# Kernel optimization log

Measured on AMD Instinct MI355X. Metric: run time of the kernel, lower is better.

Reference implementation:

```python
import jax, jax.numpy as jnp
import numpy as np

N = 50000
E = 800000
IN_F = 128
HID = 128
OUT_F = 64
MU = 2.0
EPS = 1e-12


def setup_inputs() -> dict:
    key = jax.random.key(0)
    ks = jax.random.split(key, 20)
    d = {}
    d["x"] = jax.random.normal(ks[0], (N, IN_F), dtype=jnp.float32)
    d["edge_src"] = jax.random.randint(ks[1], (E,), 0, N, dtype=jnp.int32)
    d["edge_dst"] = jax.random.randint(ks[2], (E,), 0, N, dtype=jnp.int32)
    d["edge_val"] = jax.random.uniform(ks[3], (E,), dtype=jnp.float32)
    # layer 0: in=128 -> pool=128 -> out=128 (activation=relu)
    s0 = 1.0 / np.sqrt(IN_F)
    d["pool_w0"] = jax.random.uniform(ks[4], (IN_F, IN_F), jnp.float32, -s0, s0)
    d["pool_b0"] = jax.random.uniform(ks[5], (IN_F,), jnp.float32, -s0, s0)
    d["fc1_w0"] = jax.random.uniform(ks[6], (HID, IN_F), jnp.float32, -s0, s0)
    d["fc1_b0"] = jax.random.uniform(ks[7], (HID,), jnp.float32, -s0, s0)
    d["fc2_w0"] = jax.random.uniform(ks[8], (HID, IN_F), jnp.float32, -s0, s0)
    d["fc2_b0"] = jax.random.uniform(ks[9], (HID,), jnp.float32, -s0, s0)
    # layer 1 (final): in=128 -> pool=128 -> out=64 (no activation)
    s1 = 1.0 / np.sqrt(HID)
    d["pool_w1"] = jax.random.uniform(ks[10], (HID, HID), jnp.float32, -s1, s1)
    d["pool_b1"] = jax.random.uniform(ks[11], (HID,), jnp.float32, -s1, s1)
    d["fc1_w1"] = jax.random.uniform(ks[12], (OUT_F, HID), jnp.float32, -s1, s1)
    d["fc1_b1"] = jax.random.uniform(ks[13], (OUT_F,), jnp.float32, -s1, s1)
    d["fc2_w1"] = jax.random.uniform(ks[14], (OUT_F, HID), jnp.float32, -s1, s1)
    d["fc2_b1"] = jax.random.uniform(ks[15], (OUT_F,), jnp.float32, -s1, s1)
    return d


def _sage_conv(x, src, dst, val, pw, pb, w1, b1, w2, b2, act):
    # L2-normalize rows (F.normalize(x, dim=1))
    xn = x / jnp.maximum(jnp.linalg.norm(x, axis=1, keepdims=True), EPS)
    h = jax.nn.relu(xn @ pw.T + pb)               # [N, pool]
    h_mu = h ** MU                                # elementwise pow
    # spmm(adj, h_mu): gather source rows, scale by edge weight, scatter-add to dst rows
    agg = jax.ops.segment_sum(h_mu[src] * val[:, None], dst, num_segments=N)
    agg = agg ** (1.0 / MU)                       # generalized-mean root
    out = (h @ w1.T + b1) + (agg @ w2.T + b2)
    return jax.nn.relu(out) if act else out


def reference(x, edge_src, edge_dst, edge_val,
              pool_w0, pool_b0, fc1_w0, fc1_b0, fc2_w0, fc2_b0,
              pool_w1, pool_b1, fc1_w1, fc1_b1, fc2_w1, fc2_b1):
    h = _sage_conv(x, edge_src, edge_dst, edge_val,
                   pool_w0, pool_b0, fc1_w0, fc1_b0, fc2_w0, fc2_b0, act=True)
    out = _sage_conv(h, edge_src, edge_dst, edge_val,
                     pool_w1, pool_b1, fc1_w1, fc1_b1, fc2_w1, fc2_b1, act=False)
    return out
```

## Files before the change

kernel.cpp:

```cpp
#include <hip/hip_runtime.h>

#define FF 128
#define BCAP 8192
#define CHUNK 4096
#define PITCH 136

typedef __attribute__((ext_vector_type(8))) short short8;
typedef __attribute__((ext_vector_type(4))) float f32x4;

__device__ __forceinline__ unsigned short bf16_rne(float f) {
    unsigned u = __float_as_uint(f);
    u += 0x7fffu + ((u >> 16) & 1u);
    return (unsigned short)(u >> 16);
}
__device__ __forceinline__ float bf16_to_f32(unsigned short h) {
    return __uint_as_float(((unsigned)h) << 16);
}

__global__ __launch_bounds__(256, 2)
void poolpartA_kernel(const float* __restrict__ x,
                      const unsigned short* __restrict__ Wh, const unsigned short* __restrict__ Wl,
                      const float* __restrict__ bias,
                      unsigned short* __restrict__ hout, unsigned short* __restrict__ hsqout,
                      const int* __restrict__ esrc, const int* __restrict__ edst,
                      const float* __restrict__ eval,
                      int* __restrict__ bucket_cnt, int2* __restrict__ ebuf,
                      int N, int E, int nchunks)
{
    __shared__ alignas(16) char smem[37888];
    const int t = threadIdx.x;

    if (blockIdx.x < nchunks) {
        int* cnt   = (int*)smem;
        int* sc    = cnt + 256;
        int* excl  = sc + 256;
        int* cur   = excl + 256;
        int* gbase = cur + 256;
        int2* staged = (int2*)(smem + 5 * 256 * 4);
        const int e0 = blockIdx.x * CHUNK;
        const int n  = min(CHUNK, E - e0);

        cnt[t] = 0;
        __syncthreads();
        for (int i = t; i < n; i += 256)
            atomicAdd(&cnt[((unsigned)edst[e0 + i]) >> 8], 1);
        __syncthreads();

        sc[t] = cnt[t];
        __syncthreads();
        #pragma unroll
        for (int off = 1; off < 256; off <<= 1) {
            int v = (t >= off) ? sc[t - off] : 0;
            __syncthreads();
            sc[t] += v;
            __syncthreads();
        }
        excl[t] = sc[t] - cnt[t];
        cur[t]  = excl[t];
        if (cnt[t] > 0) gbase[t] = atomicAdd(&bucket_cnt[t], cnt[t]);
        __syncthreads();

        for (int i = t; i < n; i += 256) {
            int d = edst[e0 + i];
            int s = esrc[e0 + i];
            float v = eval[e0 + i];
            int b = ((unsigned)d) >> 8;
            int slot = atomicAdd(&cur[b], 1);
            staged[slot] = make_int2((s & 0xffff) | (d << 16), __float_as_int(v));
        }
        __syncthreads();

        for (int p = t; p < n; p += 256) {
            int2 ent = staged[p];
            int b = ((unsigned)ent.x) >> 24;
            int gpos = gbase[b] + (p - excl[b]);
            ebuf[(size_t)b * BCAP + gpos] = ent;
        }
    } else {
        unsigned short* sX = (unsigned short*)smem;
        float* sNorm = (float*)(smem + 64 * PITCH * 2);
        unsigned short* sOutQ = (unsigned short*)(smem + 64 * PITCH * 2 + 256);
        const int tile = blockIdx.x - nchunks;

        #pragma unroll
        for (int rg = 0; rg < 2; ++rg) {
            const int row = rg * 32 + (t >> 3);
            const int c0  = (t & 7) * 16;
            const int n   = tile * 64 + row;
            const int base = row * PITCH + c0;
            float v[16];
            if (n < N) {
                const float4* p = (const float4*)(x + (size_t)n * FF + c0);
                #pragma unroll
                for (int i = 0; i < 4; ++i) {
                    float4 q = p[i];
                    v[4*i] = q.x; v[4*i+1] = q.y; v[4*i+2] = q.z; v[4*i+3] = q.w;
                }
            } else {
                #pragma unroll
                for (int i = 0; i < 16; ++i) v[i] = 0.f;
            }
            float ss = 0.f;
            #pragma unroll
            for (int i = 0; i < 16; ++i) ss = fmaf(v[i], v[i], ss);
            union { unsigned short u[8]; short8 s; } h0, h1;
            #pragma unroll
            for (int i = 0; i < 8; ++i) {
                h0.u[i] = bf16_rne(v[i]);
                h1.u[i] = bf16_rne(v[8 + i]);
            }
            *(short8*)&sX[base]     = h0.s;
            *(short8*)&sX[base + 8] = h1.s;
            ss += __shfl_xor(ss, 1);
            ss += __shfl_xor(ss, 2);
            ss += __shfl_xor(ss, 4);
            if ((t & 7) == 0) sNorm[row] = 1.0f / fmaxf(sqrtf(ss), 1e-12f);
        }
        __syncthreads();

        const int lane = t & 63, wave = t >> 6;
        const int quad = lane >> 4, l16 = lane & 15;

        short8 Bh[2][4], Bl[2][4];
        #pragma unroll
        for (int c = 0; c < 2; ++c) {
            const int jt = 2 * wave + c;
            #pragma unroll
            for (int tt = 0; tt < 4; ++tt) {
                const size_t o = ((size_t)(jt * 4 + tt) * 64 + lane) * 8;
                Bh[c][tt] = *(const short8*)&Wh[o];
                Bl[c][tt] = *(const short8*)&Wl[o];
            }
        }

        f32x4 acc[4][2];
        #pragma unroll
        for (int r = 0; r < 4; ++r)
            #pragma unroll
            for (int c = 0; c < 2; ++c) {
                f32x4 z = {0.f, 0.f, 0.f, 0.f};
                acc[r][c] = z;
            }

        #pragma unroll
        for (int tt = 0; tt < 4; ++tt) {
            short8 Ah[4];
            #pragma unroll
            for (int r = 0; r < 4; ++r)
                Ah[r] = *(const short8*)&sX[(r * 16 + l16) * PITCH + tt * 32 + quad * 8];
            #pragma unroll
            for (int c = 0; c < 2; ++c)
                #pragma unroll
                for (int r = 0; r < 4; ++r) {
                    acc[r][c] = __builtin_amdgcn_mfma_f32_16x16x32_bf16(Ah[r], Bh[c][tt], acc[r][c], 0, 0, 0);
                    acc[r][c] = __builtin_amdgcn_mfma_f32_16x16x32_bf16(Ah[r], Bl[c][tt], acc[r][c], 0, 0, 0);
                }
        }

        __syncthreads();
        #pragma unroll
        for (int c = 0; c < 2; ++c) {
            const int j = (2 * wave + c) * 16 + l16;
            const float bj = bias[j];
            #pragma unroll
            for (int r = 0; r < 4; ++r) {
                #pragma unroll
                for (int g = 0; g < 4; ++g) {
                    const int nl = r * 16 + quad * 4 + g;
                    float s = sNorm[nl];
                    float val = fmaf(acc[r][c][g], s, bj);
                    val = fmaxf(val, 0.f);
                    sX   [nl * PITCH + j] = bf16_rne(val);
                    sOutQ[nl * PITCH + j] = bf16_rne(val * val);
                }
            }
        }
        __syncthreads();
        #pragma unroll
        for (int rg = 0; rg < 2; ++rg) {
            const int row = rg * 32 + (t >> 3);
            const int c0  = (t & 7) * 16;
            const int n   = tile * 64 + row;
            if (n < N) {
                const int base = row * PITCH + c0;
                *(short8*)&hout  [(size_t)n * FF + c0]     = *(short8*)&sX[base];
                *(short8*)&hout  [(size_t)n * FF + c0 + 8] = *(short8*)&sX[base + 8];
                *(short8*)&hsqout[(size_t)n * FF + c0]     = *(short8*)&sOutQ[base];
                *(short8*)&hsqout[(size_t)n * FF + c0 + 8] = *(short8*)&sOutQ[base + 8];
            }
        }
    }
}

struct WPack {
    const float* src[6];
    unsigned short* hi[6];
    unsigned short* lo[6];
    int n[6];
};

__global__ __launch_bounds__(256)
void wprep_kernel(WPack p, int* __restrict__ bucket_cnt)
{
    if (blockIdx.x == 0) bucket_cnt[threadIdx.x] = 0;
    int id = blockIdx.x * 256 + threadIdx.x;
    #pragma unroll
    for (int i = 0; i < 6; ++i) {
        if (id < p.n[i]) {
            float f = p.src[i][id];
            unsigned short h = bf16_rne(f);
            const int j = id >> 7, k = id & 127;
            const int jt = j >> 4, l16 = j & 15;
            const int t = k >> 5, quad = (k >> 3) & 3, j8 = k & 7;
            const size_t o = ((size_t)((jt * 4 + t) * 4 + quad) * 16 + l16) * 8 + j8;
            p.hi[i][o] = h;
            p.lo[i][o] = bf16_rne(f - bf16_to_f32(h));
            return;
        }
        id -= p.n[i];
    }
}

__global__ __launch_bounds__(256)
void partB_kernel(const int* __restrict__ bucket_cnt, const int2* __restrict__ ebuf,
                  int* __restrict__ offsets, int2* __restrict__ edata,
                  int N, int E, int nbuck)
{
    __shared__ int pre[256], hist[256], sc[256], excl[256], cur[256];
    const int t = threadIdx.x;
    const int b = blockIdx.x;

    pre[t] = (t < nbuck) ? bucket_cnt[t] : 0;
    __syncthreads();
    #pragma unroll
    for (int off = 1; off < 256; off <<= 1) {
        int v = (t >= off) ? pre[t - off] : 0;
        __syncthreads();
        pre[t] += v;
        __syncthreads();
    }
    const int base = (b == 0) ? 0 : pre[b - 1];
    const int cnt  = pre[b] - base;

    hist[t] = 0;
    __syncthreads();
    const int2* ib = ebuf + (size_t)b * BCAP;
    for (int i = t; i < cnt; i += 256)
        atomicAdd(&hist[(((unsigned)ib[i].x) >> 16) & 255], 1);
    __syncthreads();

    sc[t] = hist[t];
    __syncthreads();
    #pragma unroll
    for (int off = 1; off < 256; off <<= 1) {
        int v = (t >= off) ? sc[t - off] : 0;
        __syncthreads();
        sc[t] += v;
        __syncthreads();
    }
    excl[t] = sc[t] - hist[t];
    cur[t]  = excl[t];

    const int node = b * 256 + t;
    if (node <= N) offsets[node] = base + excl[t];
    __syncthreads();

    for (int i = t; i < cnt; i += 256) {
        int2 ent = ib[i];
        int l = (((unsigned)ent.x) >> 16) & 255;
        int pos = base + atomicAdd(&cur[l], 1);
        edata[pos] = make_int2(ent.x & 0xffff, ent.y);
    }
}

__device__ __forceinline__ void fma4(float4& a, float v, uint2 u) {
    a.x = fmaf(v, __uint_as_float(u.x << 16), a.x);
    a.y = fmaf(v, __uint_as_float(u.x & 0xffff0000u), a.y);
    a.z = fmaf(v, __uint_as_float(u.y << 16), a.z);
    a.w = fmaf(v, __uint_as_float(u.y & 0xffff0000u), a.w);
}

__global__ __launch_bounds__(256)
void agg_kernel(const unsigned short* __restrict__ hsq, const int* __restrict__ offsets,
                const int2* __restrict__ edata,
                unsigned short* __restrict__ aggh, int N)
{
    const int w = blockIdx.x * 8 + (threadIdx.x >> 5);
    if (w >= N) return;
    const int l = threadIdx.x & 31;
    const size_t fo = (size_t)(l * 4);
    int e = offsets[w];
    const int end = offsets[w + 1];

    float4 a0 = {0,0,0,0}, a1 = {0,0,0,0}, a2 = {0,0,0,0}, a3 = {0,0,0,0};

    if ((e & 1) && e < end) {
        int2 ed = edata[e];
        uint2 u = *(const uint2*)&hsq[(size_t)ed.x * FF + fo];
        fma4(a0, __int_as_float(ed.y), u);
        ++e;
    }
    for (; e + 7 < end; e += 8) {
        int4 p0 = *(const int4*)&edata[e];
        int4 p1 = *(const int4*)&edata[e + 2];
        int4 p2 = *(const int4*)&edata[e + 4];
        int4 p3 = *(const int4*)&edata[e + 6];
        uint2 u0 = *(const uint2*)&hsq[(size_t)p0.x * FF + fo];
        uint2 u1 = *(const uint2*)&hsq[(size_t)p0.z * FF + fo];
        uint2 u2 = *(const uint2*)&hsq[(size_t)p1.x * FF + fo];
        uint2 u3 = *(const uint2*)&hsq[(size_t)p1.z * FF + fo];
        uint2 u4 = *(const uint2*)&hsq[(size_t)p2.x * FF + fo];
        uint2 u5 = *(const uint2*)&hsq[(size_t)p2.z * FF + fo];
        uint2 u6 = *(const uint2*)&hsq[(size_t)p3.x * FF + fo];
        uint2 u7 = *(const uint2*)&hsq[(size_t)p3.z * FF + fo];
        fma4(a0, __int_as_float(p0.y), u0);
        fma4(a1, __int_as_float(p0.w), u1);
        fma4(a2, __int_as_float(p1.y), u2);
        fma4(a3, __int_as_float(p1.w), u3);
        fma4(a0, __int_as_float(p2.y), u4);
        fma4(a1, __int_as_float(p2.w), u5);
        fma4(a2, __int_as_float(p3.y), u6);
        fma4(a3, __int_as_float(p3.w), u7);
    }
    if (e + 3 < end) {
        int4 p0 = *(const int4*)&edata[e];
        int4 p1 = *(const int4*)&edata[e + 2];
        uint2 u0 = *(const uint2*)&hsq[(size_t)p0.x * FF + fo];
        uint2 u1 = *(const uint2*)&hsq[(size_t)p0.z * FF + fo];
        uint2 u2 = *(const uint2*)&hsq[(size_t)p1.x * FF + fo];
        uint2 u3 = *(const uint2*)&hsq[(size_t)p1.z * FF + fo];
        fma4(a0, __int_as_float(p0.y), u0);
        fma4(a1, __int_as_float(p0.w), u1);
        fma4(a2, __int_as_float(p1.y), u2);
        fma4(a3, __int_as_float(p1.w), u3);
        e += 4;
    }
    if (e + 1 < end) {
        int4 p = *(const int4*)&edata[e];
        uint2 u0 = *(const uint2*)&hsq[(size_t)p.x * FF + fo];
        uint2 u1 = *(const uint2*)&hsq[(size_t)p.z * FF + fo];
        fma4(a0, __int_as_float(p.y), u0);
        fma4(a1, __int_as_float(p.w), u1);
        e += 2;
    }
    if (e < end) {
        int2 ed = edata[e];
        uint2 u = *(const uint2*)&hsq[(size_t)ed.x * FF + fo];
        fma4(a0, __int_as_float(ed.y), u);
    }

    float4 r;
    r.x = sqrtf(a0.x + a1.x + a2.x + a3.x);
    r.y = sqrtf(a0.y + a1.y + a2.y + a3.y);
    r.z = sqrtf(a0.z + a1.z + a2.z + a3.z);
    r.w = sqrtf(a0.w + a1.w + a2.w + a3.w);

    uint2 hv = { (unsigned)bf16_rne(r.x) | ((unsigned)bf16_rne(r.y) << 16),
                 (unsigned)bf16_rne(r.z) | ((unsigned)bf16_rne(r.w) << 16) };
    *(uint2*)&aggh[(size_t)w * FF + fo] = hv;
}

__global__ __launch_bounds__(256, 2)
void mm2pool_kernel(const unsigned short* __restrict__ hin,
                    const unsigned short* __restrict__ aggh,
                    const unsigned short* __restrict__ W1h, const unsigned short* __restrict__ W1l,
                    const unsigned short* __restrict__ W2h, const unsigned short* __restrict__ W2l,
                    const float* __restrict__ b1, const float* __restrict__ b2,
                    const unsigned short* __restrict__ PWh, const unsigned short* __restrict__ PWl,
                    const float* __restrict__ pb,
                    unsigned short* __restrict__ hout, unsigned short* __restrict__ hsqout,
                    int N)
{
    __shared__ unsigned short sH [64 * PITCH];
    __shared__ unsigned short sA [64 * PITCH];
    __shared__ unsigned short sX1[64 * PITCH];
    __shared__ float sNorm[64];

    const int tid  = threadIdx.x;
    const int tile = blockIdx.x;

    #pragma unroll
    for (int rg = 0; rg < 2; ++rg) {
        const int row = rg * 32 + (tid >> 3);
        const int c0  = (tid & 7) * 16;
        const int n   = tile * 64 + row;
        const int base = row * PITCH + c0;
        short8 z = {0,0,0,0,0,0,0,0};
        short8 a = z, b = z, c = z, d = z;
        if (n < N) {
            const short8* ph = (const short8*)(hin  + (size_t)n * FF + c0);
            const short8* pa = (const short8*)(aggh + (size_t)n * FF + c0);
            a = ph[0]; b = ph[1];
            c = pa[0]; d = pa[1];
        }
        *(short8*)&sH[base]     = a;
        *(short8*)&sH[base + 8] = b;
        *(short8*)&sA[base]     = c;
        *(short8*)&sA[base + 8] = d;
    }
    __syncthreads();

    const int lane = tid & 63, wave = tid >> 6;
    const int quad = lane >> 4, l16 = lane & 15;

    short8 B1hf[2][4], B1lf[2][4], B2hf[2][4], B2lf[2][4];
    #pragma unroll
    for (int c = 0; c < 2; ++c) {
        const int jt = 2 * wave + c;
        #pragma unroll
        for (int t = 0; t < 4; ++t) {
            const size_t o = ((size_t)(jt * 4 + t) * 64 + lane) * 8;
            B1hf[c][t] = *(const short8*)&W1h[o];
            B1lf[c][t] = *(const short8*)&W1l[o];
            B2hf[c][t] = *(const short8*)&W2h[o];
            B2lf[c][t] = *(const short8*)&W2l[o];
        }
    }

    f32x4 acc[4][2];
    #pragma unroll
    for (int r = 0; r < 4; ++r)
        #pragma unroll
        for (int c = 0; c < 2; ++c) {
            f32x4 z = {0.f, 0.f, 0.f, 0.f};
            acc[r][c] = z;
        }

    #pragma unroll
    for (int t = 0; t < 4; ++t) {
        short8 Hf[4], AH[4];
        #pragma unroll
        for (int r = 0; r < 4; ++r) {
            const int off = (r * 16 + l16) * PITCH + t * 32 + quad * 8;
            Hf[r] = *(const short8*)&sH[off];
            AH[r] = *(const short8*)&sA[off];
        }
        #pragma unroll
        for (int c = 0; c < 2; ++c)
            #pragma unroll
            for (int r = 0; r < 4; ++r) {
                acc[r][c] = __builtin_amdgcn_mfma_f32_16x16x32_bf16(Hf[r], B1hf[c][t], acc[r][c], 0, 0, 0);
                acc[r][c] = __builtin_amdgcn_mfma_f32_16x16x32_bf16(Hf[r], B1lf[c][t], acc[r][c], 0, 0, 0);
                acc[r][c] = __builtin_amdgcn_mfma_f32_16x16x32_bf16(AH[r], B2hf[c][t], acc[r][c], 0, 0, 0);
                acc[r][c] = __builtin_amdgcn_mfma_f32_16x16x32_bf16(AH[r], B2lf[c][t], acc[r][c], 0, 0, 0);
            }
    }

    #pragma unroll
    for (int c = 0; c < 2; ++c) {
        const int j = (2 * wave + c) * 16 + l16;
        const float bj = b1[j] + b2[j];
        #pragma unroll
        for (int r = 0; r < 4; ++r) {
            #pragma unroll
            for (int g = 0; g < 4; ++g) {
                const int nl = r * 16 + quad * 4 + g;
                float val = fmaxf(acc[r][c][g] + bj, 0.f);
                sX1[nl * PITCH + j] = bf16_rne(val);
            }
        }
    }
    __syncthreads();

    #pragma unroll
    for (int rg = 0; rg < 2; ++rg) {
        const int row = rg * 32 + (tid >> 3);
        const int c0  = (tid & 7) * 16;
        union { short8 s; unsigned short u[8]; } a, b;
        a.s = *(short8*)&sX1[row * PITCH + c0];
        b.s = *(short8*)&sX1[row * PITCH + c0 + 8];
        float ss = 0.f;
        #pragma unroll
        for (int i = 0; i < 8; ++i) {
            float fa = bf16_to_f32(a.u[i]);
            float fb = bf16_to_f32(b.u[i]);
            ss = fmaf(fa, fa, fmaf(fb, fb, ss));
        }
        ss += __shfl_xor(ss, 1);
        ss += __shfl_xor(ss, 2);
        ss += __shfl_xor(ss, 4);
        if ((tid & 7) == 0) sNorm[row] = 1.0f / fmaxf(sqrtf(ss), 1e-12f);
    }
    __syncthreads();

    short8 Ph[2][4], Pl[2][4];
    #pragma unroll
    for (int c = 0; c < 2; ++c) {
        const int jt = 2 * wave + c;
        #pragma unroll
        for (int t = 0; t < 4; ++t) {
            const size_t o = ((size_t)(jt * 4 + t) * 64 + lane) * 8;
            Ph[c][t] = *(const short8*)&PWh[o];
            Pl[c][t] = *(const short8*)&PWl[o];
        }
    }

    f32x4 acc2[4][2];
    #pragma unroll
    for (int r = 0; r < 4; ++r)
        #pragma unroll
        for (int c = 0; c < 2; ++c) {
            f32x4 z = {0.f, 0.f, 0.f, 0.f};
            acc2[r][c] = z;
        }

    #pragma unroll
    for (int t = 0; t < 4; ++t) {
        short8 Ah[4];
        #pragma unroll
        for (int r = 0; r < 4; ++r)
            Ah[r] = *(const short8*)&sX1[(r * 16 + l16) * PITCH + t * 32 + quad * 8];
        #pragma unroll
        for (int c = 0; c < 2; ++c)
            #pragma unroll
            for (int r = 0; r < 4; ++r) {
                acc2[r][c] = __builtin_amdgcn_mfma_f32_16x16x32_bf16(Ah[r], Ph[c][t], acc2[r][c], 0, 0, 0);
                acc2[r][c] = __builtin_amdgcn_mfma_f32_16x16x32_bf16(Ah[r], Pl[c][t], acc2[r][c], 0, 0, 0);
            }
    }

    __syncthreads();
    #pragma unroll
    for (int c = 0; c < 2; ++c) {
        const int j = (2 * wave + c) * 16 + l16;
        const float pbj = pb[j];
        #pragma unroll
        for (int r = 0; r < 4; ++r) {
            #pragma unroll
            for (int g = 0; g < 4; ++g) {
                const int nl = r * 16 + quad * 4 + g;
                float s = sNorm[nl];
                float val = fmaxf(fmaf(acc2[r][c][g], s, pbj), 0.f);
                sH[nl * PITCH + j] = bf16_rne(val);
                sA[nl * PITCH + j] = bf16_rne(val * val);
            }
        }
    }
    __syncthreads();
    #pragma unroll
    for (int rg = 0; rg < 2; ++rg) {
        const int row = rg * 32 + (tid >> 3);
        const int c0  = (tid & 7) * 16;
        const int n   = tile * 64 + row;
        if (n < N) {
            const int base = row * PITCH + c0;
            *(short8*)&hout  [(size_t)n * FF + c0]     = *(short8*)&sH[base];
            *(short8*)&hout  [(size_t)n * FF + c0 + 8] = *(short8*)&sH[base + 8];
            *(short8*)&hsqout[(size_t)n * FF + c0]     = *(short8*)&sA[base];
            *(short8*)&hsqout[(size_t)n * FF + c0 + 8] = *(short8*)&sA[base + 8];
        }
    }
}

#define OPITCH 68
__global__ __launch_bounds__(256, 2)
void mm2_final_kernel(const unsigned short* __restrict__ hin,
                      const unsigned short* __restrict__ aggh,
                      const unsigned short* __restrict__ W1h, const unsigned short* __restrict__ W1l,
                      const unsigned short* __restrict__ W2h, const unsigned short* __restrict__ W2l,
                      const float* __restrict__ b1, const float* __restrict__ b2,
                      float* __restrict__ out, int N)
{
    __shared__ unsigned short sH[64 * PITCH];
    __shared__ unsigned short sA[64 * PITCH];

    const int tid  = threadIdx.x;
    const int tile = blockIdx.x;

    #pragma unroll
    for (int rg = 0; rg < 2; ++rg) {
        const int row = rg * 32 + (tid >> 3);
        const int c0  = (tid & 7) * 16;
        const int n   = tile * 64 + row;
        const int base = row * PITCH + c0;
        short8 z = {0,0,0,0,0,0,0,0};
        short8 a = z, b = z, c = z, d = z;
        if (n < N) {
            const short8* ph = (const short8*)(hin  + (size_t)n * FF + c0);
            const short8* pa = (const short8*)(aggh + (size_t)n * FF + c0);
            a = ph[0]; b = ph[1];
            c = pa[0]; d = pa[1];
        }
        *(short8*)&sH[base]     = a;
        *(short8*)&sH[base + 8] = b;
        *(short8*)&sA[base]     = c;
        *(short8*)&sA[base + 8] = d;
    }
    __syncthreads();

    const int lane = tid & 63, wave = tid >> 6;
    const int quad = lane >> 4, l16 = lane & 15;

    short8 B1hf[4], B1lf[4], B2hf[4], B2lf[4];
    #pragma unroll
    for (int t = 0; t < 4; ++t) {
        const size_t o = ((size_t)(wave * 4 + t) * 64 + lane) * 8;
        B1hf[t] = *(const short8*)&W1h[o];
        B1lf[t] = *(const short8*)&W1l[o];
        B2hf[t] = *(const short8*)&W2h[o];
        B2lf[t] = *(const short8*)&W2l[o];
    }

    f32x4 acc[4];
    #pragma unroll
    for (int r = 0; r < 4; ++r) {
        f32x4 z = {0.f, 0.f, 0.f, 0.f};
        acc[r] = z;
    }

    #pragma unroll
    for (int t = 0; t < 4; ++t) {
        short8 Hf[4], AH[4];
        #pragma unroll
        for (int r = 0; r < 4; ++r) {
            const int off = (r * 16 + l16) * PITCH + t * 32 + quad * 8;
            Hf[r] = *(const short8*)&sH[off];
            AH[r] = *(const short8*)&sA[off];
        }
        #pragma unroll
        for (int r = 0; r < 4; ++r) {
            acc[r] = __builtin_amdgcn_mfma_f32_16x16x32_bf16(Hf[r], B1hf[t], acc[r], 0, 0, 0);
            acc[r] = __builtin_amdgcn_mfma_f32_16x16x32_bf16(Hf[r], B1lf[t], acc[r], 0, 0, 0);
            acc[r] = __builtin_amdgcn_mfma_f32_16x16x32_bf16(AH[r], B2hf[t], acc[r], 0, 0, 0);
            acc[r] = __builtin_amdgcn_mfma_f32_16x16x32_bf16(AH[r], B2lf[t], acc[r], 0, 0, 0);
        }
    }

    __syncthreads();
    float* sOut = (float*)sH;
    {
        const int j = wave * 16 + l16;
        const float bj = b1[j] + b2[j];
        #pragma unroll
        for (int r = 0; r < 4; ++r) {
            #pragma unroll
            for (int g = 0; g < 4; ++g) {
                const int nl = r * 16 + quad * 4 + g;
                sOut[nl * OPITCH + j] = acc[r][g] + bj;
            }
        }
    }
    __syncthreads();
    {
        const int row = tid >> 2;
        const int seg = tid & 3;
        const int n = tile * 64 + row;
        if (n < N) {
            const float4* src = (const float4*)&sOut[row * OPITCH + seg * 16];
            float4* dst = (float4*)&out[(size_t)n * 64 + seg * 16];
            #pragma unroll
            for (int i = 0; i < 4; ++i) dst[i] = src[i];
        }
    }
}

extern "C" void kernel_launch(void* const* d_in, const int* in_sizes, int n_in,
                              void* d_out, int out_size, void* d_ws, size_t ws_size,
                              hipStream_t stream) {
    const float* x    = (const float*)d_in[0];
    const int*   esrc = (const int*)d_in[1];
    const int*   edst = (const int*)d_in[2];
    const float* eval = (const float*)d_in[3];
    const float* pw0  = (const float*)d_in[4];
    const float* pb0  = (const float*)d_in[5];
    const float* f1w0 = (const float*)d_in[6];
    const float* f1b0 = (const float*)d_in[7];
    const float* f2w0 = (const float*)d_in[8];
    const float* f2b0 = (const float*)d_in[9];
    const float* pw1  = (const float*)d_in[10];
    const float* pb1  = (const float*)d_in[11];
    const float* f1w1 = (const float*)d_in[12];
    const float* f1b1 = (const float*)d_in[13];
    const float* f2w1 = (const float*)d_in[14];
    const float* f2b1 = (const float*)d_in[15];
    float* out = (float*)d_out;

    const int N = in_sizes[0] / FF;
    const int E = in_sizes[1];
    const int nbuck = (N + 255) / 256;

    char* ws = (char*)d_ws;
    const size_t planesz = (size_t)N * FF * 2;
    const size_t A = 256;
    size_t off = 0;
    unsigned short* h    = (unsigned short*)(ws + off); off += (planesz + A - 1) / A * A;
    unsigned short* hsq  = (unsigned short*)(ws + off); off += (planesz + A - 1) / A * A;
    unsigned short* h2   = (unsigned short*)(ws + off); off += (planesz + A - 1) / A * A;
    unsigned short* hsq2 = (unsigned short*)(ws + off); off += (planesz + A - 1) / A * A;
    unsigned short* aggh = (unsigned short*)(ws + off); off += (planesz + A - 1) / A * A;
    int* offsets = (int*)(ws + off); off += ((size_t)(N + 1) * 4 + A - 1) / A * A;
    int* bucket_cnt = (int*)(ws + off); off += (size_t)256 * 4;
    int2* ebuf  = (int2*)(ws + off); off += (size_t)nbuck * BCAP * 8;
    int2* edata = (int2*)(ws + off); off += (size_t)E * 8;
    const int wsz[6] = {128 * FF, 128 * FF, 128 * FF, 128 * FF, 64 * FF, 64 * FF};
    unsigned short* whi[6];
    unsigned short* wlo[6];
    for (int i = 0; i < 6; ++i) {
        whi[i] = (unsigned short*)(ws + off); off += (size_t)wsz[i] * 2;
        wlo[i] = (unsigned short*)(ws + off); off += (size_t)wsz[i] * 2;
    }

    WPack pack;
    const float* wsrc[6] = {pw0, f1w0, f2w0, pw1, f1w1, f2w1};
    int wtotal = 0;
    for (int i = 0; i < 6; ++i) {
        pack.src[i] = wsrc[i]; pack.hi[i] = whi[i]; pack.lo[i] = wlo[i]; pack.n[i] = wsz[i];
        wtotal += wsz[i];
    }

    const int ntiles     = (N + 63) / 64;
    const int nodeblocks = (N + 7) / 8;
    const int nchunks    = (E + CHUNK - 1) / CHUNK;
    dim3 B(256);

    wprep_kernel<<<(wtotal + 255) / 256, B, 0, stream>>>(pack, bucket_cnt);

    poolpartA_kernel<<<nchunks + ntiles, B, 0, stream>>>(
        x, whi[0], wlo[0], pb0, h, hsq, esrc, edst, eval, bucket_cnt, ebuf, N, E, nchunks);

    partB_kernel<<<nbuck, B, 0, stream>>>(bucket_cnt, ebuf, offsets, edata, N, E, nbuck);

    agg_kernel<<<nodeblocks, B, 0, stream>>>(hsq, offsets, edata, aggh, N);

    mm2pool_kernel<<<ntiles, B, 0, stream>>>(
        h, aggh, whi[1], wlo[1], whi[2], wlo[2], f1b0, f2b0,
        whi[3], wlo[3], pb1, h2, hsq2, N);

    agg_kernel<<<nodeblocks, B, 0, stream>>>(hsq2, offsets, edata, aggh, N);

    mm2_final_kernel<<<ntiles, B, 0, stream>>>(
        h2, aggh, whi[4], wlo[4], whi[5], wlo[5], f1b1, f2b1, out, N);
}
```

Before: 234.8 us.

## Process two nodes per warp in aggregation, pad bucket counters, register-cache edges

The aggregation kernel now gives each 32-lane group two destination nodes and interleaves their gathers, which raises memory-level parallelism and halves the grid. Partition A loads each edge once into registers instead of reading edst/esrc/eval twice. Bucket counters are spaced BSTRIDE ints apart so the global atomics on different buckets land in separate cache lines. The costs are higher register pressure and uneven work when the two nodes have different degrees.

```diff
diff --git a/kernel.cpp b/kernel.cpp
--- a/kernel.cpp
+++ b/kernel.cpp
@@ -4,6 +4,7 @@
 #define BCAP 8192
 #define CHUNK 4096
 #define PITCH 136
+#define BSTRIDE 32
 
 typedef __attribute__((ext_vector_type(8))) short short8;
 typedef __attribute__((ext_vector_type(4))) float f32x4;
@@ -40,10 +41,24 @@
         const int e0 = blockIdx.x * CHUNK;
         const int n  = min(CHUNK, E - e0);
 
+        unsigned pk[16]; float vr[16];
+        #pragma unroll
+        for (int k = 0; k < 16; ++k) {
+            const int i = t + k * 256;
+            pk[k] = 0xFFFFFFFFu;
+            if (i < n) {
+                int d = edst[e0 + i];
+                int s = esrc[e0 + i];
+                pk[k] = (unsigned)((s & 0xffff) | (d << 16));
+                vr[k] = eval[e0 + i];
+            }
+        }
+
         cnt[t] = 0;
         __syncthreads();
-        for (int i = t; i < n; i += 256)
-            atomicAdd(&cnt[((unsigned)edst[e0 + i]) >> 8], 1);
+        #pragma unroll
+        for (int k = 0; k < 16; ++k)
+            if (pk[k] != 0xFFFFFFFFu) atomicAdd(&cnt[pk[k] >> 24], 1);
         __syncthreads();
 
         sc[t] = cnt[t];
@@ -57,16 +72,16 @@
         }
         excl[t] = sc[t] - cnt[t];
         cur[t]  = excl[t];
-        if (cnt[t] > 0) gbase[t] = atomicAdd(&bucket_cnt[t], cnt[t]);
-        __syncthreads();
-
-        for (int i = t; i < n; i += 256) {
-            int d = edst[e0 + i];
-            int s = esrc[e0 + i];
-            float v = eval[e0 + i];
-            int b = ((unsigned)d) >> 8;
-            int slot = atomicAdd(&cur[b], 1);
-            staged[slot] = make_int2((s & 0xffff) | (d << 16), __float_as_int(v));
+        if (cnt[t] > 0) gbase[t] = atomicAdd(&bucket_cnt[t * BSTRIDE], cnt[t]);
+        __syncthreads();
+
+        #pragma unroll
+        for (int k = 0; k < 16; ++k) {
+            if (pk[k] != 0xFFFFFFFFu) {
+                int b = pk[k] >> 24;
+                int slot = atomicAdd(&cur[b], 1);
+                staged[slot] = make_int2((int)pk[k], __float_as_int(vr[k]));
+            }
         }
         __syncthreads();
 
@@ -202,7 +217,9 @@
 __global__ __launch_bounds__(256)
 void wprep_kernel(WPack p, int* __restrict__ bucket_cnt)
 {
-    if (blockIdx.x == 0) bucket_cnt[threadIdx.x] = 0;
+    if (blockIdx.x == 0) {
+        for (int i = threadIdx.x; i < 256 * BSTRIDE; i += 256) bucket_cnt[i] = 0;
+    }
     int id = blockIdx.x * 256 + threadIdx.x;
     #pragma unroll
     for (int i = 0; i < 6; ++i) {
@@ -230,7 +247,7 @@
     const int t = threadIdx.x;
     const int b = blockIdx.x;
 
-    pre[t] = (t < nbuck) ? bucket_cnt[t] : 0;
+    pre[t] = (t < nbuck) ? bucket_cnt[t * BSTRIDE] : 0;
     __syncthreads();
     #pragma unroll
     for (int off = 1; off < 256; off <<= 1) {
@@ -285,79 +302,130 @@
                 const int2* __restrict__ edata,
                 unsigned short* __restrict__ aggh, int N)
 {
-    const int w = blockIdx.x * 8 + (threadIdx.x >> 5);
-    if (w >= N) return;
+    const int g  = blockIdx.x * 8 + (threadIdx.x >> 5);
+    const int w0 = g * 2;
+    if (w0 >= N) return;
+    const int w1 = w0 + 1;
+    const bool has1 = (w1 < N);
     const int l = threadIdx.x & 31;
     const size_t fo = (size_t)(l * 4);
-    int e = offsets[w];
-    const int end = offsets[w + 1];
-
-    float4 a0 = {0,0,0,0}, a1 = {0,0,0,0}, a2 = {0,0,0,0}, a3 = {0,0,0,0};
-
-    if ((e & 1) && e < end) {
-        int2 ed = edata[e];
+
+    int e0 = offsets[w0];
+    const int end0 = offsets[w0 + 1];
+    int e1 = end0;
+    const int end1 = has1 ? offsets[w1 + 1] : end0;
+
+    float4 x0 = {0,0,0,0}, y0 = {0,0,0,0};
+    float4 x1 = {0,0,0,0}, y1 = {0,0,0,0};
+
+    if ((e0 & 1) && e0 < end0) {
+        int2 ed = edata[e0];
         uint2 u = *(const uint2*)&hsq[(size_t)ed.x * FF + fo];
-        fma4(a0, __int_as_float(ed.y), u);
-        ++e;
-    }
-    for (; e + 7 < end; e += 8) {
-        int4 p0 = *(const int4*)&edata[e];
-        int4 p1 = *(const int4*)&edata[e + 2];
-        int4 p2 = *(const int4*)&edata[e + 4];
-        int4 p3 = *(const int4*)&edata[e + 6];
-        uint2 u0 = *(const uint2*)&hsq[(size_t)p0.x * FF + fo];
-        uint2 u1 = *(const uint2*)&hsq[(size_t)p0.z * FF + fo];
-        uint2 u2 = *(const uint2*)&hsq[(size_t)p1.x * FF + fo];
-        uint2 u3 = *(const uint2*)&hsq[(size_t)p1.z * FF + fo];
-        uint2 u4 = *(const uint2*)&hsq[(size_t)p2.x * FF + fo];
-        uint2 u5 = *(const uint2*)&hsq[(size_t)p2.z * FF + fo];
-        uint2 u6 = *(const uint2*)&hsq[(size_t)p3.x * FF + fo];
-        uint2 u7 = *(const uint2*)&hsq[(size_t)p3.z * FF + fo];
-        fma4(a0, __int_as_float(p0.y), u0);
-        fma4(a1, __int_as_float(p0.w), u1);
-        fma4(a2, __int_as_float(p1.y), u2);
-        fma4(a3, __int_as_float(p1.w), u3);
-        fma4(a0, __int_as_float(p2.y), u4);
-        fma4(a1, __int_as_float(p2.w), u5);
-        fma4(a2, __int_as_float(p3.y), u6);
-        fma4(a3, __int_as_float(p3.w), u7);
-    }
-    if (e + 3 < end) {
-        int4 p0 = *(const int4*)&edata[e];
-        int4 p1 = *(const int4*)&edata[e + 2];
-        uint2 u0 = *(const uint2*)&hsq[(size_t)p0.x * FF + fo];
-        uint2 u1 = *(const uint2*)&hsq[(size_t)p0.z * FF + fo];
-        uint2 u2 = *(const uint2*)&hsq[(size_t)p1.x * FF + fo];
-        uint2 u3 = *(const uint2*)&hsq[(size_t)p1.z * FF + fo];
-        fma4(a0, __int_as_float(p0.y), u0);
-        fma4(a1, __int_as_float(p0.w), u1);
-        fma4(a2, __int_as_float(p1.y), u2);
-        fma4(a3, __int_as_float(p1.w), u3);
-        e += 4;
-    }
-    if (e + 1 < end) {
-        int4 p = *(const int4*)&edata[e];
-        uint2 u0 = *(const uint2*)&hsq[(size_t)p.x * FF + fo];
-        uint2 u1 = *(const uint2*)&hsq[(size_t)p.z * FF + fo];
-        fma4(a0, __int_as_float(p.y), u0);
-        fma4(a1, __int_as_float(p.w), u1);
-        e += 2;
-    }
-    if (e < end) {
-        int2 ed = edata[e];
+        fma4(x0, __int_as_float(ed.y), u);
+        ++e0;
+    }
+    if ((e1 & 1) && e1 < end1) {
+        int2 ed = edata[e1];
         uint2 u = *(const uint2*)&hsq[(size_t)ed.x * FF + fo];
-        fma4(a0, __int_as_float(ed.y), u);
-    }
-
-    float4 r;
-    r.x = sqrtf(a0.x + a1.x + a2.x + a3.x);
-    r.y = sqrtf(a0.y + a1.y + a2.y + a3.y);
-    r.z = sqrtf(a0.z + a1.z + a2.z + a3.z);
-    r.w = sqrtf(a0.w + a1.w + a2.w + a3.w);
-
-    uint2 hv = { (unsigned)bf16_rne(r.x) | ((unsigned)bf16_rne(r.y) << 16),
-                 (unsigned)bf16_rne(r.z) | ((unsigned)bf16_rne(r.w) << 16) };
-    *(uint2*)&aggh[(size_t)w * FF + fo] = hv;
+        fma4(x1, __int_as_float(ed.y), u);
+        ++e1;
+    }
+
+    while (e0 + 3 < end0 && e1 + 3 < end1) {
+        int4 p00 = *(const int4*)&edata[e0];
+        int4 p01 = *(const int4*)&edata[e0 + 2];
+        int4 p10 = *(const int4*)&edata[e1];
+        int4 p11 = *(const int4*)&edata[e1 + 2];
+        uint2 u00 = *(const uint2*)&hsq[(size_t)p00.x * FF + fo];
+        uint2 u01 = *(const uint2*)&hsq[(size_t)p00.z * FF + fo];
+        uint2 u02 = *(const uint2*)&hsq[(size_t)p01.x * FF + fo];
+        uint2 u03 = *(const uint2*)&hsq[(size_t)p01.z * FF + fo];
+        uint2 u10 = *(const uint2*)&hsq[(size_t)p10.x * FF + fo];
+        uint2 u11 = *(const uint2*)&hsq[(size_t)p10.z * FF + fo];
+        uint2 u12 = *(const uint2*)&hsq[(size_t)p11.x * FF + fo];
+        uint2 u13 = *(const uint2*)&hsq[(size_t)p11.z * FF + fo];
+        fma4(x0, __int_as_float(p00.y), u00);
+        fma4(y0, __int_as_float(p00.w), u01);
+        fma4(x0, __int_as_float(p01.y), u02);
+        fma4(y0, __int_as_float(p01.w), u03);
+        fma4(x1, __int_as_float(p10.y), u10);
+        fma4(y1, __int_as_float(p10.w), u11);
+        fma4(x1, __int_as_float(p11.y), u12);
+        fma4(y1, __int_as_float(p11.w), u13);
+        e0 += 4; e1 += 4;
+    }
+
+    for (; e0 + 3 < end0; e0 += 4) {
+        int4 pa = *(const int4*)&edata[e0];
+        int4 pb = *(const int4*)&edata[e0 + 2];
+        uint2 ua = *(const uint2*)&hsq[(size_t)pa.x * FF + fo];
+        uint2 ub = *(const uint2*)&hsq[(size_t)pa.z * FF + fo];
+        uint2 uc = *(const uint2*)&hsq[(size_t)pb.x * FF + fo];
+        uint2 ud = *(const uint2*)&hsq[(size_t)pb.z * FF + fo];
+        fma4(x0, __int_as_float(pa.y), ua);
+        fma4(y0, __int_as_float(pa.w), ub);
+        fma4(x0, __int_as_float(pb.y), uc);
+        fma4(y0, __int_as_float(pb.w), ud);
+    }
+    if (e0 + 1 < end0) {
+        int4 p = *(const int4*)&edata[e0];
+        uint2 ua = *(const uint2*)&hsq[(size_t)p.x * FF + fo];
+        uint2 ub = *(const uint2*)&hsq[(size_t)p.z * FF + fo];
+        fma4(x0, __int_as_float(p.y), ua);
+        fma4(y0, __int_as_float(p.w), ub);
+        e0 += 2;
+    }
+    if (e0 < end0) {
+        int2 ed = edata[e0];
+        uint2 u = *(const uint2*)&hsq[(size_t)ed.x * FF + fo];
+        fma4(x0, __int_as_float(ed.y), u);
+    }
+
+    for (; e1 + 3 < end1; e1 += 4) {
+        int4 pa = *(const int4*)&edata[e1];
+        int4 pb = *(const int4*)&edata[e1 + 2];
+        uint2 ua = *(const uint2*)&hsq[(size_t)pa.x * FF + fo];
+        uint2 ub = *(const uint2*)&hsq[(size_t)pa.z * FF + fo];
+        uint2 uc = *(const uint2*)&hsq[(size_t)pb.x * FF + fo];
+        uint2 ud = *(const uint2*)&hsq[(size_t)pb.z * FF + fo];
+        fma4(x1, __int_as_float(pa.y), ua);
+        fma4(y1, __int_as_float(pa.w), ub);
+        fma4(x1, __int_as_float(pb.y), uc);
+        fma4(y1, __int_as_float(pb.w), ud);
+    }
+    if (e1 + 1 < end1) {
+        int4 p = *(const int4*)&edata[e1];
+        uint2 ua = *(const uint2*)&hsq[(size_t)p.x * FF + fo];
+        uint2 ub = *(const uint2*)&hsq[(size_t)p.z * FF + fo];
+        fma4(x1, __int_as_float(p.y), ua);
+        fma4(y1, __int_as_float(p.w), ub);
+        e1 += 2;
+    }
+    if (e1 < end1) {
+        int2 ed = edata[e1];
+        uint2 u = *(const uint2*)&hsq[(size_t)ed.x * FF + fo];
+        fma4(x1, __int_as_float(ed.y), u);
+    }
+
+    float4 r0;
+    r0.x = sqrtf(x0.x + y0.x);
+    r0.y = sqrtf(x0.y + y0.y);
+    r0.z = sqrtf(x0.z + y0.z);
+    r0.w = sqrtf(x0.w + y0.w);
+    uint2 h0 = { (unsigned)bf16_rne(r0.x) | ((unsigned)bf16_rne(r0.y) << 16),
+                 (unsigned)bf16_rne(r0.z) | ((unsigned)bf16_rne(r0.w) << 16) };
+    *(uint2*)&aggh[(size_t)w0 * FF + fo] = h0;
+
+    if (has1) {
+        float4 r1;
+        r1.x = sqrtf(x1.x + y1.x);
+        r1.y = sqrtf(x1.y + y1.y);
+        r1.z = sqrtf(x1.z + y1.z);
+        r1.w = sqrtf(x1.w + y1.w);
+        uint2 h1 = { (unsigned)bf16_rne(r1.x) | ((unsigned)bf16_rne(r1.y) << 16),
+                     (unsigned)bf16_rne(r1.z) | ((unsigned)bf16_rne(r1.w) << 16) };
+        *(uint2*)&aggh[(size_t)w1 * FF + fo] = h1;
+    }
 }
 
 __global__ __launch_bounds__(256, 2)
@@ -689,7 +757,7 @@
     unsigned short* hsq2 = (unsigned short*)(ws + off); off += (planesz + A - 1) / A * A;
     unsigned short* aggh = (unsigned short*)(ws + off); off += (planesz + A - 1) / A * A;
     int* offsets = (int*)(ws + off); off += ((size_t)(N + 1) * 4 + A - 1) / A * A;
-    int* bucket_cnt = (int*)(ws + off); off += (size_t)256 * 4;
+    int* bucket_cnt = (int*)(ws + off); off += (size_t)256 * BSTRIDE * 4;
     int2* ebuf  = (int2*)(ws + off); off += (size_t)nbuck * BCAP * 8;
     int2* edata = (int2*)(ws + off); off += (size_t)E * 8;
     const int wsz[6] = {128 * FF, 128 * FF, 128 * FF, 128 * FF, 64 * FF, 64 * FF};
@@ -709,7 +777,7 @@
     }
 
     const int ntiles     = (N + 63) / 64;
-    const int nodeblocks = (N + 7) / 8;
+    const int nodeblocks = (N + 15) / 16;
     const int nchunks    = (E + CHUNK - 1) / CHUNK;
     dim3 B(256);
 
```

New measurement: 240.1 us. +2.3%, slower.
